# Kernel tuning notes

Hardware: AMD Instinct MI355X
Metric: run time of the kernel (lower is better)

## Reference

```python
import jax, jax.numpy as jnp
import numpy as np

B = 128        # graph pairs per batch
NPG = 512      # nodes per graph (equal-size graphs -> dense batch is a reshape)
D = 64         # input feature dim
DEG = 16       # avg degree
FILTERS = [64, 32, 16]
RDIM = 10      # resize_dim
CCH = 8        # conv channels per similarity image
MLP = [32, 16, 8, 4, 1]


def _make_edges(rng, n_graphs, npg, deg):
    E = n_graphs * npg * deg
    off = np.repeat(np.arange(n_graphs, dtype=np.int64) * npg, npg * deg)
    src = rng.integers(0, npg, E) + off
    dst = rng.integers(0, npg, E) + off
    return jnp.asarray(np.stack([src, dst]), dtype=jnp.int32)


def setup_inputs() -> dict:
    key = jax.random.key(0)
    ks = jax.random.split(key, 40)
    rng = np.random.default_rng(0)
    N = B * NPG
    inp = {}
    inp['x_i'] = jax.random.normal(ks[0], (N, D), jnp.float32)
    inp['x_j'] = jax.random.normal(ks[1], (N, D), jnp.float32)
    # GCN weights
    dims = [D] + FILTERS
    k = 2
    for li in range(3):
        fi, fo = dims[li], dims[li + 1]
        inp[f'gcn_w{li}'] = jax.random.normal(ks[k], (fi, fo), jnp.float32) / np.sqrt(fi); k += 1
        inp[f'gcn_b{li}'] = jnp.zeros((fo,), jnp.float32)
    # Conv filters: one Conv2d(1->CCH, 3x3, SAME) per GNN layer, OIHW kernels
    for li in range(3):
        inp[f'conv_w{li}'] = jax.random.normal(ks[k], (CCH, 1, 3, 3), jnp.float32) / 3.0; k += 1
        inp[f'conv_b{li}'] = jnp.zeros((CCH,), jnp.float32)
    # MLP (Linear-ReLU stack) + scoring layer
    mdims = [3 * CCH * RDIM * RDIM] + MLP
    for li in range(len(MLP)):
        fi, fo = mdims[li], mdims[li + 1]
        inp[f'mlp_w{li}'] = jax.random.normal(ks[k], (fi, fo), jnp.float32) / np.sqrt(fi); k += 1
        inp[f'mlp_b{li}'] = jnp.zeros((fo,), jnp.float32)
    inp['score_w'] = jax.random.normal(ks[k], (1, 1), jnp.float32); k += 1
    inp['score_b'] = jnp.zeros((1,), jnp.float32)
    # Graph structure (int constants)
    inp['edge_index_i'] = _make_edges(rng, B, NPG, DEG)
    inp['edge_index_j'] = _make_edges(rng, B, NPG, DEG)
    batch = jnp.asarray(np.repeat(np.arange(B, dtype=np.int64), NPG), dtype=jnp.int32)
    inp['batch_i'] = batch
    inp['batch_j'] = batch
    return inp


def _gcn(x, ei, w, b):
    # PyG GCNConv: A_hat = D^-1/2 (A + I) D^-1/2 ; out = A_hat (x W) + b
    src, dst = ei[0], ei[1]
    n = x.shape[0]
    xw = x @ w
    deg = jax.ops.segment_sum(jnp.ones(ei.shape[1], xw.dtype), dst, num_segments=n) + 1.0
    inv = jax.lax.rsqrt(deg)
    msg = xw[src] * (inv[src] * inv[dst])[:, None]
    agg = jax.ops.segment_sum(msg, dst, num_segments=n)
    return agg + xw * (inv * inv)[:, None] + b


def _forward(x_i, x_j, gcn_w0, gcn_b0, gcn_w1, gcn_b1, gcn_w2, gcn_b2,
             conv_w0, conv_b0, conv_w1, conv_b1, conv_w2, conv_b2,
             mlp_w0, mlp_b0, mlp_w1, mlp_b1, mlp_w2, mlp_b2, mlp_w3, mlp_b3, mlp_w4, mlp_b4,
             score_w, score_b, edge_index_i, edge_index_j):
    gws = [(gcn_w0, gcn_b0), (gcn_w1, gcn_b1), (gcn_w2, gcn_b2)]
    cvs = [(conv_w0, conv_b0), (conv_w1, conv_b1), (conv_w2, conv_b2)]
    embs = []
    for li, (w, b) in enumerate(gws):
        x_i = _gcn(x_i, edge_index_i, w, b)
        x_j = _gcn(x_j, edge_index_j, w, b)
        if li != len(gws) - 1:  # activation + dropout (eval mode -> identity)
            x_i = jax.nn.relu(x_i)
            x_j = jax.nn.relu(x_j)
        h_i = x_i.reshape(B, NPG, -1)  # to_dense_batch (equal-size graphs)
        h_j = x_j.reshape(B, NPG, -1)
        sim = jnp.einsum('bnd,bmd->bnm', h_i, h_j)  # [B, NPG, NPG]
        simr = jax.image.resize(sim, (B, RDIM, RDIM), method='bilinear', antialias=False)
        cw, cb = cvs[li]
        y = jax.lax.conv_general_dilated(simr[:, None], cw, (1, 1), 'SAME')
        y = jax.nn.relu(y + cb[None, :, None, None])  # [B, CCH, RDIM, RDIM]
        embs.append(y.reshape(B, -1))
    feat = jnp.concatenate(embs, axis=1)  # [B, 3*CCH*RDIM*RDIM]
    for w, b in [(mlp_w0, mlp_b0), (mlp_w1, mlp_b1), (mlp_w2, mlp_b2), (mlp_w3, mlp_b3), (mlp_w4, mlp_b4)]:
        feat = jax.nn.relu(feat @ w + b)
    score = jax.nn.sigmoid(feat @ score_w + score_b)
    return score.reshape(-1)


def reference(x_i, x_j, gcn_w0, gcn_b0, gcn_w1, gcn_b1, gcn_w2, gcn_b2,
              conv_w0, conv_b0, conv_w1, conv_b1, conv_w2, conv_b2,
              mlp_w0, mlp_b0, mlp_w1, mlp_b1, mlp_w2, mlp_b2, mlp_w3, mlp_b3, mlp_w4, mlp_b4,
              score_w, score_b, edge_index_i, edge_index_j, batch_i, batch_j):
    # batch_i/batch_j are implicit in the block layout (equal-size graphs)
    return _forward(x_i, x_j, gcn_w0, gcn_b0, gcn_w1, gcn_b1, gcn_w2, gcn_b2,
                    conv_w0, conv_b0, conv_w1, conv_b1, conv_w2, conv_b2,
                    mlp_w0, mlp_b0, mlp_w1, mlp_b1, mlp_w2, mlp_b2, mlp_w3, mlp_b3, mlp_w4, mlp_b4,
                    score_w, score_b, edge_index_i, edge_index_j)
```

## Files before the change

kernel.cpp:

```cpp
#include <hip/hip_runtime.h>

typedef float fvec4 __attribute__((ext_vector_type(4)));

#define NN 65536
#define EE 1048576
#define BB 128
#define NPG 512
#define EPG 8192

template <int FOUT, bool RELU, bool LAST>
__device__ __forceinline__ void agg_chunk(const fvec4 (&acc)[4], fvec4 (&o)[4], int c,
                                          const float* __restrict__ bias,
                                          int start, int count, float inv_v, int slot,
                                          fvec4* __restrict__ msgQ, const int* __restrict__ sids,
                                          float* __restrict__ hs, int hb) {
  const int v = threadIdx.x;
  {
    const int lb = (v >> 1) << 3;
    const int m = ((v & 1) << 2) + ((v >> 1) & 7);
#pragma unroll
    for (int q = 0; q < 4; ++q) msgQ[lb + ((q + m) & 7)] = acc[q] * inv_v;
  }
  __syncthreads();
  if (!LAST || slot >= 0) {
    fvec4 s0 = {0.f, 0.f, 0.f, 0.f}, s1 = s0, s2 = s0, s3 = s0;
    int e = start;
    const int end = start + count;
#define ACC_EDGE(P) { const int m_ = (P) & 15; const int l_ = ((P) >> 4) << 3;       \
      s0 += msgQ[l_ + (m_ & 7)];       s1 += msgQ[l_ + ((1 + m_) & 7)];              \
      s2 += msgQ[l_ + ((2 + m_) & 7)]; s3 += msgQ[l_ + ((3 + m_) & 7)]; }
    for (; e + 2 <= end; e += 2) {
      const int a0 = sids[e], a1 = sids[e + 1];
      ACC_EDGE(a0) ACC_EDGE(a1)
    }
    if (e < end) { const int a0 = sids[e]; ACC_EDGE(a0) }
#undef ACC_EDGE
    fvec4 sArr[4] = {s0, s1, s2, s3};
    const float i2 = inv_v * inv_v;
#pragma unroll
    for (int q = 0; q < 4; ++q) {
#pragma unroll
      for (int j = 0; j < 4; ++j) {
        float ov = sArr[q][j] * inv_v + acc[q][j] * i2 + bias[c * 16 + q * 4 + j];
        if (RELU) ov = fmaxf(ov, 0.f);
        o[q][j] = ov;
      }
    }
    if (slot >= 0) {
      fvec4* hp = reinterpret_cast<fvec4*>(hs + ((size_t)hb + slot) * FOUT + c * 16);
#pragma unroll
      for (int q = 0; q < 4; ++q) hp[q] = o[q];
    }
  }
  __syncthreads();
}

__global__ __launch_bounds__(512)
void k_all(const float* __restrict__ x_i, const float* __restrict__ x_j,
           const float* __restrict__ gw0, const float* __restrict__ gb0,
           const float* __restrict__ gw1, const float* __restrict__ gb1,
           const float* __restrict__ gw2, const float* __restrict__ gb2,
           const int* __restrict__ ei, const int* __restrict__ ej,
           float* __restrict__ hs0, float* __restrict__ hs1, float* __restrict__ hs2) {
  __shared__ int sids[EPG];
  __shared__ fvec4 msgQ[8 * (NPG / 2)];
  __shared__ int cnt[NPG];
  __shared__ int posb[NPG];
  __shared__ int wsum[8];
  int* const dsts = reinterpret_cast<int*>(msgQ);

  const int side = blockIdx.x >> 7;
  const int g = blockIdx.x & 127;
  const float* __restrict__ x = side ? x_j : x_i;
  const int* __restrict__ eidx = side ? ej : ei;
  const int v = threadIdx.x;
  const int base = g * NPG;
  const int ebase = g * EPG;

  cnt[v] = 0;
  __syncthreads();
  for (int k = v; k < EPG; k += 512) {
    int d = eidx[EE + ebase + k] - base;
    dsts[k] = d;
    atomicAdd(&cnt[d], 1);
  }
  __syncthreads();

  const int count = cnt[v];
  int xa = count;
  const int lane = v & 63;
#pragma unroll
  for (int d = 1; d < 64; d <<= 1) {
    int y = __shfl_up(xa, d, 64);
    if (lane >= d) xa += y;
  }
  const int wid = v >> 6;
  if (lane == 63) wsum[wid] = xa;
  __syncthreads();
  if (v == 0) {
    int a = 0;
#pragma unroll
    for (int i = 0; i < 8; ++i) { int tv = wsum[i]; wsum[i] = a; a += tv; }
  }
  __syncthreads();
  const int start = xa - count + wsum[wid];
  posb[v] = start;
  const float inv_v = rsqrtf((float)count + 1.0f);
  __syncthreads();

  for (int k = v; k < EPG; k += 512) {
    int sv = eidx[ebase + k] - base;
    int p = atomicAdd(&posb[dsts[k]], 1);
    int line = sv >> 1;
    int m = ((sv & 1) << 2) + (line & 7);
    sids[p] = (line << 4) | m;
  }
  __syncthreads();

  constexpr int srows[20] = {25, 26, 76, 77, 127, 128, 178, 179, 229, 230,
                             281, 282, 332, 333, 383, 384, 434, 435, 485, 486};
  int slot = -1;
#pragma unroll
  for (int i = 0; i < 20; ++i)
    if (v == srows[i]) slot = i;
  const int hb = (side * BB + g) * 20;

  fvec4 a0[16];
#pragma unroll
  for (int q = 0; q < 16; ++q) a0[q] = fvec4{0.f, 0.f, 0.f, 0.f};
  {
    const fvec4* xv = reinterpret_cast<const fvec4*>(x + (size_t)(base + v) * 64);
#pragma unroll 1
    for (int k16 = 0; k16 < 4; ++k16) {
      fvec4 xq[4];
#pragma unroll
      for (int u = 0; u < 4; ++u) xq[u] = xv[4 * k16 + u];
#pragma unroll
      for (int u = 0; u < 4; ++u) {
#pragma unroll
        for (int j = 0; j < 4; ++j) {
          const float xk = xq[u][j];
          const fvec4* wr = reinterpret_cast<const fvec4*>(gw0 + (size_t)(16 * k16 + 4 * u + j) * 64);
#pragma unroll
          for (int q = 0; q < 16; ++q) a0[q] += xk * wr[q];
        }
      }
    }
  }

  fvec4 y1[8];
#pragma unroll
  for (int c = 0; c < 4; ++c) {
    fvec4 acc[4], o[4];
#pragma unroll
    for (int q = 0; q < 4; ++q) acc[q] = a0[4 * c + q];
    agg_chunk<64, true, false>(acc, o, c, gb0, start, count, inv_v, slot, msgQ, sids, hs0, hb);
    if (c == 0) {
#pragma unroll
      for (int q = 0; q < 8; ++q) y1[q] = fvec4{0.f, 0.f, 0.f, 0.f};
    }
#pragma unroll
    for (int f = 0; f < 16; ++f) {
      const float hf = o[f >> 2][f & 3];
      const fvec4* wr = reinterpret_cast<const fvec4*>(gw1 + (size_t)(16 * c + f) * 32);
#pragma unroll
      for (int q = 0; q < 8; ++q) y1[q] += hf * wr[q];
    }
  }

  fvec4 y2[4];
#pragma unroll
  for (int c = 0; c < 2; ++c) {
    fvec4 acc[4], o[4];
#pragma unroll
    for (int q = 0; q < 4; ++q) acc[q] = y1[4 * c + q];
    agg_chunk<32, true, false>(acc, o, c, gb1, start, count, inv_v, slot, msgQ, sids, hs1, hb);
    if (c == 0) {
#pragma unroll
      for (int q = 0; q < 4; ++q) y2[q] = fvec4{0.f, 0.f, 0.f, 0.f};
    }
#pragma unroll
    for (int f = 0; f < 16; ++f) {
      const float hf = o[f >> 2][f & 3];
      const fvec4* wr = reinterpret_cast<const fvec4*>(gw2 + (size_t)(16 * c + f) * 16);
#pragma unroll
      for (int q = 0; q < 4; ++q) y2[q] += hf * wr[q];
    }
  }

  {
    fvec4 o[4];
    agg_chunk<16, false, true>(y2, o, 0, gb2, start, count, inv_v, slot, msgQ, sids, hs2, hb);
  }
}

__global__ __launch_bounds__(256) void k_head(const float* __restrict__ hs0, const float* __restrict__ hs1,
                                              const float* __restrict__ hs2,
                                              const float* __restrict__ cw0, const float* __restrict__ cb0,
                                              const float* __restrict__ cw1, const float* __restrict__ cb1,
                                              const float* __restrict__ cw2, const float* __restrict__ cb2,
                                              const float* __restrict__ mw0, const float* __restrict__ mb0,
                                              const float* __restrict__ mw1, const float* __restrict__ mb1,
                                              const float* __restrict__ mw2, const float* __restrict__ mb2,
                                              const float* __restrict__ mw3, const float* __restrict__ mb3,
                                              const float* __restrict__ mw4, const float* __restrict__ mb4,
                                              const float* __restrict__ sw, const float* __restrict__ sb,
                                              float* __restrict__ out) {
  __shared__ float hi[2240];
  __shared__ float hj[2240];
  __shared__ float sim[400];
  __shared__ float simr[100];
  __shared__ float feat[2400];
  __shared__ float red[256];
  __shared__ float mbuf[60];
  const int b = blockIdx.x, t = threadIdx.x;

  for (int k = t; k < 1280; k += 256) {
    hi[k] = hs0[(size_t)(0 * BB + b) * 1280 + k];
    hj[k] = hs0[(size_t)(1 * BB + b) * 1280 + k];
  }
  for (int k = t; k < 640; k += 256) {
    hi[1280 + k] = hs1[(size_t)(0 * BB + b) * 640 + k];
    hj[1280 + k] = hs1[(size_t)(1 * BB + b) * 640 + k];
  }
  for (int k = t; k < 320; k += 256) {
    hi[1920 + k] = hs2[(size_t)(0 * BB + b) * 320 + k];
    hj[1920 + k] = hs2[(size_t)(1 * BB + b) * 320 + k];
  }
  __syncthreads();

  const int Fs[3] = {64, 32, 16};
  const int HOFF[3] = {0, 1280, 1920};
  const float* CW[3] = {cw0, cw1, cw2};
  const float* CB[3] = {cb0, cb1, cb2};

  for (int li = 0; li < 3; ++li) {
    const int F = Fs[li];
    const float* Hi = hi + HOFF[li];
    const float* Hj = hj + HOFF[li];
    for (int p = t; p < 400; p += 256) {
      int r = p / 20, cq = p % 20;
      float a = 0.0f;
      for (int d = 0; d < F; ++d) a += Hi[r * F + d] * Hj[cq * F + d];
      sim[p] = a;
    }
    __syncthreads();
    if (t < 100) {
      int oy = t / 10, ox = t % 10;
      float cy = (oy + 0.5f) * (512.0f / 10.0f) - 0.5f;
      float cx = (ox + 0.5f) * (512.0f / 10.0f) - 0.5f;
      float fy = cy - floorf(cy);
      float fx = cx - floorf(cx);
      int r0 = 2 * oy, c0 = 2 * ox;
      float s00 = sim[r0 * 20 + c0], s01 = sim[r0 * 20 + c0 + 1];
      float s10 = sim[(r0 + 1) * 20 + c0], s11 = sim[(r0 + 1) * 20 + c0 + 1];
      simr[t] = (1.0f - fy) * ((1.0f - fx) * s00 + fx * s01) + fy * ((1.0f - fx) * s10 + fx * s11);
    }
    __syncthreads();
    const float* cw = CW[li];
    const float* cb = CB[li];
    for (int idx = t; idx < 800; idx += 256) {
      int cch = idx / 100, rem = idx % 100, y = rem / 10, x = rem % 10;
      float a = cb[cch];
#pragma unroll
      for (int ky = 0; ky < 3; ++ky) {
#pragma unroll
        for (int kx = 0; kx < 3; ++kx) {
          int iy = y + ky - 1, ix = x + kx - 1;
          if (iy >= 0 && iy < 10 && ix >= 0 && ix < 10)
            a += cw[cch * 9 + ky * 3 + kx] * simr[iy * 10 + ix];
        }
      }
      feat[li * 800 + idx] = fmaxf(a, 0.0f);
    }
    __syncthreads();
  }

  {
    int f = t & 31, part = t >> 5;
    float a = 0.0f;
    int k0 = part * 300;
    for (int k = k0; k < k0 + 300; ++k) a += feat[k] * mw0[k * 32 + f];
    red[t] = a;
    __syncthreads();
    if (t < 32) {
      float s = mb0[t];
#pragma unroll
      for (int p = 0; p < 8; ++p) s += red[p * 32 + t];
      mbuf[t] = fmaxf(s, 0.0f);
    }
    __syncthreads();
  }
  if (t < 16) {
    float s = mb1[t];
    for (int k = 0; k < 32; ++k) s += mbuf[k] * mw1[k * 16 + t];
    mbuf[32 + t] = fmaxf(s, 0.0f);
  }
  __syncthreads();
  if (t < 8) {
    float s = mb2[t];
    for (int k = 0; k < 16; ++k) s += mbuf[32 + k] * mw2[k * 8 + t];
    mbuf[48 + t] = fmaxf(s, 0.0f);
  }
  __syncthreads();
  if (t < 4) {
    float s = mb3[t];
    for (int k = 0; k < 8; ++k) s += mbuf[48 + k] * mw3[k * 4 + t];
    mbuf[56 + t] = fmaxf(s, 0.0f);
  }
  __syncthreads();
  if (t == 0) {
    float s = mb4[0];
    for (int k = 0; k < 4; ++k) s += mbuf[56 + k] * mw4[k];
    s = fmaxf(s, 0.0f);
    float z = s * sw[0] + sb[0];
    out[b] = 1.0f / (1.0f + expf(-z));
  }
}

extern "C" void kernel_launch(void* const* d_in, const int* in_sizes, int n_in,
                              void* d_out, int out_size, void* d_ws, size_t ws_size,
                              hipStream_t stream) {
  (void)in_sizes; (void)n_in; (void)out_size; (void)ws_size;
  const float* x_i = (const float*)d_in[0];
  const float* x_j = (const float*)d_in[1];
  const float* gw0 = (const float*)d_in[2];
  const float* gb0 = (const float*)d_in[3];
  const float* gw1 = (const float*)d_in[4];
  const float* gb1 = (const float*)d_in[5];
  const float* gw2 = (const float*)d_in[6];
  const float* gb2 = (const float*)d_in[7];
  const float* cw0 = (const float*)d_in[8];
  const float* cb0 = (const float*)d_in[9];
  const float* cw1 = (const float*)d_in[10];
  const float* cb1 = (const float*)d_in[11];
  const float* cw2 = (const float*)d_in[12];
  const float* cb2 = (const float*)d_in[13];
  const float* mw0 = (const float*)d_in[14];
  const float* mb0 = (const float*)d_in[15];
  const float* mw1 = (const float*)d_in[16];
  const float* mb1 = (const float*)d_in[17];
  const float* mw2 = (const float*)d_in[18];
  const float* mb2 = (const float*)d_in[19];
  const float* mw3 = (const float*)d_in[20];
  const float* mb3 = (const float*)d_in[21];
  const float* mw4 = (const float*)d_in[22];
  const float* mb4 = (const float*)d_in[23];
  const float* scw = (const float*)d_in[24];
  const float* scb = (const float*)d_in[25];
  const int* ei = (const int*)d_in[26];
  const int* ej = (const int*)d_in[27];
  float* out = (float*)d_out;

  char* p = (char*)d_ws;
  auto take = [&](size_t bytes) {
    char* r = p;
    p += (bytes + 255) & ~(size_t)255;
    return r;
  };
  float* hs0 = (float*)take((size_t)2 * BB * 20 * 64 * 4);
  float* hs1 = (float*)take((size_t)2 * BB * 20 * 32 * 4);
  float* hs2 = (float*)take((size_t)2 * BB * 20 * 16 * 4);

  k_all<<<2 * BB, 512, 0, stream>>>(x_i, x_j, gw0, gb0, gw1, gb1, gw2, gb2,
                                    ei, ej, hs0, hs1, hs2);
  k_head<<<BB, 256, 0, stream>>>(hs0, hs1, hs2, cw0, cb0, cw1, cb1, cw2, cb2,
                                 mw0, mb0, mw1, mb1, mw2, mb2, mw3, mb3, mw4, mb4,
                                 scw, scb, out);
}
```

Before: 140.7 us.

## Sort nodes by degree and aggregate 32-feature chunks per shared-memory pass

Threads are reassigned to nodes sorted by in-degree through a shared histogram and prefix scan, so lanes in a wavefront run similar-length edge loops and divergence drops. The message buffer grows to a full 32 features per node, so each aggregation pass covers 32 features instead of 16. That halves the number of barriers and edge-list traversals. The cost is more shared memory (less occupancy headroom), more live registers, and extra setup work for the sort.

Measured after the change: 130.5 us. 1.08x faster.

```diff
diff --git a/kernel.cpp b/kernel.cpp
--- a/kernel.cpp
+++ b/kernel.cpp
@@ -8,48 +8,53 @@
 #define NPG 512
 #define EPG 8192
 
-template <int FOUT, bool RELU, bool LAST>
-__device__ __forceinline__ void agg_chunk(const fvec4 (&acc)[4], fvec4 (&o)[4], int c,
-                                          const float* __restrict__ bias,
-                                          int start, int count, float inv_v, int slot,
-                                          fvec4* __restrict__ msgQ, const int* __restrict__ sids,
-                                          float* __restrict__ hs, int hb) {
-  const int v = threadIdx.x;
-  {
-    const int lb = (v >> 1) << 3;
-    const int m = ((v & 1) << 2) + ((v >> 1) & 7);
-#pragma unroll
-    for (int q = 0; q < 4; ++q) msgQ[lb + ((q + m) & 7)] = acc[q] * inv_v;
+template <int NQ, int FOUT, int COFF, bool RELU, bool LAST>
+__device__ __forceinline__ void pass32(const fvec4* acc, fvec4* o,
+                                       const float* __restrict__ bias,
+                                       int node, int start, int count, float inv_v, int slot,
+                                       fvec4* __restrict__ msgQ, const int* __restrict__ sids,
+                                       float* __restrict__ hs, int hb) {
+  {
+    const int rb = node << 3;
+    const int m = node & 7;
+#pragma unroll
+    for (int q = 0; q < NQ; ++q) msgQ[rb | ((q + m) & 7)] = acc[q] * inv_v;
   }
   __syncthreads();
   if (!LAST || slot >= 0) {
-    fvec4 s0 = {0.f, 0.f, 0.f, 0.f}, s1 = s0, s2 = s0, s3 = s0;
+    fvec4 s[NQ];
+#pragma unroll
+    for (int q = 0; q < NQ; ++q) s[q] = fvec4{0.f, 0.f, 0.f, 0.f};
     int e = start;
     const int end = start + count;
-#define ACC_EDGE(P) { const int m_ = (P) & 15; const int l_ = ((P) >> 4) << 3;       \
-      s0 += msgQ[l_ + (m_ & 7)];       s1 += msgQ[l_ + ((1 + m_) & 7)];              \
-      s2 += msgQ[l_ + ((2 + m_) & 7)]; s3 += msgQ[l_ + ((3 + m_) & 7)]; }
     for (; e + 2 <= end; e += 2) {
-      const int a0 = sids[e], a1 = sids[e + 1];
-      ACC_EDGE(a0) ACC_EDGE(a1)
-    }
-    if (e < end) { const int a0 = sids[e]; ACC_EDGE(a0) }
-#undef ACC_EDGE
-    fvec4 sArr[4] = {s0, s1, s2, s3};
+      const int k0 = sids[e], k1 = sids[e + 1];
+      const int b0 = k0 & ~7, b1 = k1 & ~7;
+#pragma unroll
+      for (int q = 0; q < NQ; ++q) s[q] += msgQ[b0 | ((q + k0) & 7)];
+#pragma unroll
+      for (int q = 0; q < NQ; ++q) s[q] += msgQ[b1 | ((q + k1) & 7)];
+    }
+    if (e < end) {
+      const int k0 = sids[e];
+      const int b0 = k0 & ~7;
+#pragma unroll
+      for (int q = 0; q < NQ; ++q) s[q] += msgQ[b0 | ((q + k0) & 7)];
+    }
     const float i2 = inv_v * inv_v;
 #pragma unroll
-    for (int q = 0; q < 4; ++q) {
+    for (int q = 0; q < NQ; ++q) {
 #pragma unroll
       for (int j = 0; j < 4; ++j) {
-        float ov = sArr[q][j] * inv_v + acc[q][j] * i2 + bias[c * 16 + q * 4 + j];
+        float ov = s[q][j] * inv_v + acc[q][j] * i2 + bias[COFF + q * 4 + j];
         if (RELU) ov = fmaxf(ov, 0.f);
         o[q][j] = ov;
       }
     }
     if (slot >= 0) {
-      fvec4* hp = reinterpret_cast<fvec4*>(hs + ((size_t)hb + slot) * FOUT + c * 16);
-#pragma unroll
-      for (int q = 0; q < 4; ++q) hp[q] = o[q];
+      fvec4* hp = reinterpret_cast<fvec4*>(hs + ((size_t)hb + slot) * FOUT + COFF);
+#pragma unroll
+      for (int q = 0; q < NQ; ++q) hp[q] = o[q];
     }
   }
   __syncthreads();
@@ -63,9 +68,12 @@
            const int* __restrict__ ei, const int* __restrict__ ej,
            float* __restrict__ hs0, float* __restrict__ hs1, float* __restrict__ hs2) {
   __shared__ int sids[EPG];
-  __shared__ fvec4 msgQ[8 * (NPG / 2)];
+  __shared__ fvec4 msgQ[NPG * 8];
   __shared__ int cnt[NPG];
   __shared__ int posb[NPG];
+  __shared__ int nodeOf[NPG];
+  __shared__ int bins[64];
+  __shared__ int binpos[64];
   __shared__ int wsum[8];
   int* const dsts = reinterpret_cast<int*>(msgQ);
 
@@ -78,6 +86,7 @@
   const int ebase = g * EPG;
 
   cnt[v] = 0;
+  if (v < 64) bins[v] = 0;
   __syncthreads();
   for (int k = v; k < EPG; k += 512) {
     int d = eidx[EE + ebase + k] - base;
@@ -87,6 +96,8 @@
   __syncthreads();
 
   const int count = cnt[v];
+  const int deg = count > 63 ? 63 : count;
+  atomicAdd(&bins[deg], 1);
   int xa = count;
   const int lane = v & 63;
 #pragma unroll
@@ -97,39 +108,55 @@
   const int wid = v >> 6;
   if (lane == 63) wsum[wid] = xa;
   __syncthreads();
-  if (v == 0) {
-    int a = 0;
-#pragma unroll
-    for (int i = 0; i < 8; ++i) { int tv = wsum[i]; wsum[i] = a; a += tv; }
-  }
-  __syncthreads();
-  const int start = xa - count + wsum[wid];
-  posb[v] = start;
-  const float inv_v = rsqrtf((float)count + 1.0f);
+  if (v < 64) {
+    if (v == 0) {
+      int a = 0;
+#pragma unroll
+      for (int i = 0; i < 8; ++i) { int tv = wsum[i]; wsum[i] = a; a += tv; }
+    }
+    int c = bins[v];
+    int xb = c;
+#pragma unroll
+    for (int d = 1; d < 64; d <<= 1) {
+      int y = __shfl_up(xb, d, 64);
+      if (v >= d) xb += y;
+    }
+    binpos[v] = xb - c;
+  }
+  __syncthreads();
+  const int start_v = xa - count + wsum[wid];
+  posb[v] = start_v;
+  {
+    int rank = atomicAdd(&binpos[deg], 1);
+    nodeOf[rank] = v;
+  }
   __syncthreads();
 
   for (int k = v; k < EPG; k += 512) {
-    int sv = eidx[ebase + k] - base;
+    int lv = eidx[ebase + k] - base;
     int p = atomicAdd(&posb[dsts[k]], 1);
-    int line = sv >> 1;
-    int m = ((sv & 1) << 2) + (line & 7);
-    sids[p] = (line << 4) | m;
-  }
-  __syncthreads();
+    sids[p] = (lv << 3) | (lv & 7);
+  }
+  __syncthreads();
+
+  const int node = nodeOf[v];
+  const int ncount = cnt[node];
+  const int nstart = posb[node] - ncount;
+  const float inv_v = rsqrtf((float)ncount + 1.0f);
 
   constexpr int srows[20] = {25, 26, 76, 77, 127, 128, 178, 179, 229, 230,
                              281, 282, 332, 333, 383, 384, 434, 435, 485, 486};
   int slot = -1;
 #pragma unroll
   for (int i = 0; i < 20; ++i)
-    if (v == srows[i]) slot = i;
+    if (node == srows[i]) slot = i;
   const int hb = (side * BB + g) * 20;
 
   fvec4 a0[16];
 #pragma unroll
   for (int q = 0; q < 16; ++q) a0[q] = fvec4{0.f, 0.f, 0.f, 0.f};
   {
-    const fvec4* xv = reinterpret_cast<const fvec4*>(x + (size_t)(base + v) * 64);
+    const fvec4* xv = reinterpret_cast<const fvec4*>(x + (size_t)(base + node) * 64);
 #pragma unroll 1
     for (int k16 = 0; k16 < 4; ++k16) {
       fvec4 xq[4];
@@ -149,40 +176,41 @@
   }
 
   fvec4 y1[8];
-#pragma unroll
-  for (int c = 0; c < 4; ++c) {
-    fvec4 acc[4], o[4];
-#pragma unroll
-    for (int q = 0; q < 4; ++q) acc[q] = a0[4 * c + q];
-    agg_chunk<64, true, false>(acc, o, c, gb0, start, count, inv_v, slot, msgQ, sids, hs0, hb);
-    if (c == 0) {
-#pragma unroll
-      for (int q = 0; q < 8; ++q) y1[q] = fvec4{0.f, 0.f, 0.f, 0.f};
-    }
-#pragma unroll
-    for (int f = 0; f < 16; ++f) {
+  {
+    fvec4 o[8];
+    pass32<8, 64, 0, true, false>(&a0[0], o, gb0, node, nstart, ncount, inv_v, slot, msgQ, sids, hs0, hb);
+#pragma unroll
+    for (int q = 0; q < 8; ++q) y1[q] = fvec4{0.f, 0.f, 0.f, 0.f};
+#pragma unroll
+    for (int f = 0; f < 32; ++f) {
       const float hf = o[f >> 2][f & 3];
-      const fvec4* wr = reinterpret_cast<const fvec4*>(gw1 + (size_t)(16 * c + f) * 32);
+      const fvec4* wr = reinterpret_cast<const fvec4*>(gw1 + (size_t)f * 32);
 #pragma unroll
       for (int q = 0; q < 8; ++q) y1[q] += hf * wr[q];
     }
   }
+  {
+    fvec4 o[8];
+    pass32<8, 64, 32, true, false>(&a0[8], o, gb0, node, nstart, ncount, inv_v, slot, msgQ, sids, hs0, hb);
+#pragma unroll
+    for (int f = 0; f < 32; ++f) {
+      const float hf = o[f >> 2][f & 3];
+      const fvec4* wr = reinterpret_cast<const fvec4*>(gw1 + (size_t)(32 + f) * 32);
+#pragma unroll
+      for (int q = 0; q < 8; ++q) y1[q] += hf * wr[q];
+    }
+  }
 
   fvec4 y2[4];
-#pragma unroll
-  for (int c = 0; c < 2; ++c) {
-    fvec4 acc[4], o[4];
-#pragma unroll
-    for (int q = 0; q < 4; ++q) acc[q] = y1[4 * c + q];
-    agg_chunk<32, true, false>(acc, o, c, gb1, start, count, inv_v, slot, msgQ, sids, hs1, hb);
-    if (c == 0) {
-#pragma unroll
-      for (int q = 0; q < 4; ++q) y2[q] = fvec4{0.f, 0.f, 0.f, 0.f};
-    }
-#pragma unroll
-    for (int f = 0; f < 16; ++f) {
+  {
+    fvec4 o[8];
+    pass32<8, 32, 0, true, false>(y1, o, gb1, node, nstart, ncount, inv_v, slot, msgQ, sids, hs1, hb);
+#pragma unroll
+    for (int q = 0; q < 4; ++q) y2[q] = fvec4{0.f, 0.f, 0.f, 0.f};
+#pragma unroll
+    for (int f = 0; f < 32; ++f) {
       const float hf = o[f >> 2][f & 3];
-      const fvec4* wr = reinterpret_cast<const fvec4*>(gw2 + (size_t)(16 * c + f) * 16);
+      const fvec4* wr = reinterpret_cast<const fvec4*>(gw2 + (size_t)f * 16);
 #pragma unroll
       for (int q = 0; q < 4; ++q) y2[q] += hf * wr[q];
     }
@@ -190,7 +218,7 @@
 
   {
     fvec4 o[4];
-    agg_chunk<16, false, true>(y2, o, 0, gb2, start, count, inv_v, slot, msgQ, sids, hs2, hb);
+    pass32<4, 16, 0, false, true>(y2, o, gb2, node, nstart, ncount, inv_v, slot, msgQ, sids, hs2, hb);
   }
 }
 
```
